# Kernel tuning notes

Hardware: AMD Instinct MI355X
Metric: run time of the kernel (lower is better)

## Reference

```python
import jax, jax.numpy as jnp
import numpy as np
import math

B, CK, CV, H, W = 16, 64, 512, 56, 56


def setup_inputs() -> dict:
    key = jax.random.key(0)
    k1, k2, k3, k4 = jax.random.split(key, 4)
    return {
        "mk": jax.random.normal(k1, (B, CK, H, W), dtype=jnp.float32),
        "qk": jax.random.normal(k2, (B, CK, H, W), dtype=jnp.float32),
        "mv": jax.random.normal(k3, (B, CV, H, W), dtype=jnp.float32),
        "qv": jax.random.normal(k4, (B, CV, H, W), dtype=jnp.float32),
    }


def reference(mk, qk, mv, qv):
    b, ck, h, w = qk.shape
    cv = mv.shape[1]
    n = h * w
    qk_f = qk.reshape(b, ck, n)          # [B, CK, HW] query keys
    mk_f = mk.reshape(b, ck, -1)         # [B, CK, N_mem]
    # squared-L2 affinity (query-norm term is constant per column -> dropped, cancels in softmax)
    a = jnp.sum(mk_f * mk_f, axis=1)[:, :, None]                # [B, N_mem, 1]
    bb = 2.0 * jnp.einsum('bcn,bcm->bnm', mk_f, qk_f)           # [B, N_mem, HW]
    affinity = (-a + bb) / math.sqrt(ck)
    affinity = jax.nn.softmax(affinity, axis=1)                 # softmax over memory dim
    # readout: weighted sum of memory values
    mem = jnp.einsum('bcn,bnm->bcm', mv.reshape(b, cv, -1), affinity)
    mem = mem.reshape(b, cv, h, w)
    return mem, qv
```

## Files before the change

kernel.cpp:

```cpp
#include <hip/hip_runtime.h>


#define B_   16
#define CK_  64
#define CV_  512
#define N_   3136
#define NPAD 3200
#define TM   64
#define TN   128
#define NITER 25
#define NBLK32 100
#define NBLK16 200

typedef __bf16 bf16_t;
typedef bf16_t bf16x8 __attribute__((ext_vector_type(8)));
typedef bf16_t bf16x4 __attribute__((ext_vector_type(4)));
typedef float  f32x16 __attribute__((ext_vector_type(16)));
typedef float  f32x4  __attribute__((ext_vector_type(4)));

#define SCALE_DOT 0.36067376022224085f

__global__ __launch_bounds__(256) void prep_kq(const float* __restrict__ mk,
                                               const float* __restrict__ qk,
                                               bf16_t* __restrict__ Kf,
                                               bf16_t* __restrict__ Qf,
                                               float* __restrict__ a2) {
  int idx = blockIdx.x * 256 + threadIdx.x;
  int b = idx / NPAD, n = idx % NPAD;
  bool valid = n < N_;
  int l32n = n & 31, nblk = n >> 5;
  float ss = 0.f;
  const float* mkp = mk + (size_t)b * CK_ * N_ + n;
  const float* qkp = qk + (size_t)b * CK_ * N_ + n;
  bf16x8* Kf8 = (bf16x8*)Kf;
  bf16x8* Qf8 = (bf16x8*)Qf;
  #pragma unroll
  for (int cc = 0; cc < 8; cc++) {
    bf16x8 kv, qv8;
    #pragma unroll
    for (int j = 0; j < 8; j++) {
      int c = 8 * cc + j;
      float kx = valid ? mkp[(size_t)c * N_] : 0.f;
      float qx = valid ? qkp[(size_t)c * N_] : 0.f;
      ss += kx * kx;
      kv[j] = (bf16_t)kx;
      qv8[j] = (bf16_t)qx;
    }
    int s = cc >> 1, hh = cc & 1;
    size_t pos = (((size_t)b * NBLK32 + nblk) * 4 + s) * 64 + l32n + 32 * hh;
    Kf8[pos] = kv;
    Qf8[pos] = qv8;
  }
  a2[idx] = ss * 0.125f * 1.4426950408889634f;
}

__global__ __launch_bounds__(256) void prep_v(const float* __restrict__ mv,
                                              bf16_t* __restrict__ Vf) {
  int idx = blockIdx.x * 256 + threadIdx.x;
  int lane = idx & 63;
  int t1 = idx >> 6;
  int nblk = t1 % NBLK16;
  int t2 = t1 / NBLK16;
  int cblk = t2 & 15;
  int b = t2 >> 4;
  int c = cblk * 32 + (lane & 31);
  int n = nblk * 16 + (lane >> 5) * 8;
  bf16x8 o;
  if (n < N_) {
    const float* p = mv + ((size_t)b * CV_ + c) * N_ + n;
    f32x4 v0 = *(const f32x4*)p;
    f32x4 v1 = *(const f32x4*)(p + 4);
    #pragma unroll
    for (int j = 0; j < 4; j++) { o[j] = (bf16_t)v0[j]; o[4 + j] = (bf16_t)v1[j]; }
  } else {
    #pragma unroll
    for (int j = 0; j < 8; j++) o[j] = (bf16_t)0.f;
  }
  ((bf16x8*)Vf)[idx] = o;
}

__global__ __launch_bounds__(512) void attn_main(const bf16_t* __restrict__ Kf,
                                                 const bf16_t* __restrict__ Qf,
                                                 const float* __restrict__ a2,
                                                 const bf16_t* __restrict__ Vf,
                                                 float* __restrict__ out) {
  const int xcd = blockIdx.x & 7;
  const int idx = blockIdx.x >> 3;
  const int q49 = idx / 49;
  const int b   = xcd * 2 + q49;
  const int m0  = (idx - q49 * 49) * TM;

  const int tid  = threadIdx.x;
  const int w    = tid >> 6;
  const int lane = tid & 63;
  const int l32  = lane & 31;
  const int h    = lane >> 5;
  const int g    = w >> 2;
  const int i    = w & 3;

  __shared__ __align__(16) bf16_t Plds[2][64][128];
  __shared__ float  Llds[8][32];
  __shared__ float  Linv[64];

  const bf16x8* Qf8 = (const bf16x8*)Qf;
  const int mblk = (m0 >> 5) + g;
  bf16x8 qfrag[4];
  #pragma unroll
  for (int s = 0; s < 4; s++)
    qfrag[s] = Qf8[(((size_t)b * NBLK32 + mblk) * 4 + s) * 64 + lane];

  f32x16 acc[2][2];
  #pragma unroll
  for (int cb = 0; cb < 2; cb++)
    #pragma unroll
    for (int mb = 0; mb < 2; mb++)
      #pragma unroll
      for (int r = 0; r < 16; r++) acc[cb][mb][r] = 0.f;

  float Lpart = 0.f;
  const float*  a2b = a2 + (size_t)b * NPAD;
  const bf16x8* Kf8 = (const bf16x8*)Kf;
  const bf16x8* Vf8 = (const bf16x8*)Vf + (((size_t)b * 16 + 2 * w) * NBLK16) * 64 + lane;

  const int wrow = 32 * g + l32;
  const int wswz = (wrow & 15) << 4;
  const int rswz = (l32 & 15) << 4;

  for (int iter = 0; iter < NITER; iter++) {
    const int n0 = iter * TN + 32 * i;

    f32x16 sacc;
    #pragma unroll
    for (int r = 0; r < 16; r++) sacc[r] = 0.f;
    const bf16x8* kp = Kf8 + (((size_t)b * NBLK32 + (iter * 4 + i)) * 4) * 64 + lane;
    #pragma unroll
    for (int s = 0; s < 4; s++) {
      bf16x8 kf = kp[s * 64];
      sacc = __builtin_amdgcn_mfma_f32_32x32x16_bf16(kf, qfrag[s], sacc, 0, 0, 0);
    }

    char* Pb = (char*)Plds[iter & 1];
    #pragma unroll
    for (int t = 0; t < 4; t++) {
      bf16x4 pk;
      #pragma unroll
      for (int q = 0; q < 4; q++) {
        int r = 8 * t + 4 * h + q;
        int n = n0 + r;
        float vv = sacc[4 * t + q] * SCALE_DOT - a2b[n];
        float p = (n < N_) ? __builtin_amdgcn_exp2f(vv) : 0.f;
        Lpart += p;
        pk[q] = (bf16_t)p;
      }
      int colb = 64 * i + 16 * t + 8 * h;
      *(bf16x4*)(Pb + wrow * 256 + (colb ^ wswz)) = pk;
    }

    __syncthreads();

    const bf16x8* vp = Vf8 + (size_t)iter * 8 * 64;
    #pragma unroll
    for (int t = 0; t < 8; t++) {
      bf16x8 vf0 = vp[t * 64];
      bf16x8 vf1 = vp[t * 64 + 12800];
      bf16x8 pf0 = *(const bf16x8*)(Pb + l32 * 256 + ((32 * t + 16 * h) ^ rswz));
      bf16x8 pf1 = *(const bf16x8*)(Pb + (32 + l32) * 256 + ((32 * t + 16 * h) ^ rswz));
      acc[0][0] = __builtin_amdgcn_mfma_f32_32x32x16_bf16(vf0, pf0, acc[0][0], 0, 0, 0);
      acc[0][1] = __builtin_amdgcn_mfma_f32_32x32x16_bf16(vf0, pf1, acc[0][1], 0, 0, 0);
      acc[1][0] = __builtin_amdgcn_mfma_f32_32x32x16_bf16(vf1, pf0, acc[1][0], 0, 0, 0);
      acc[1][1] = __builtin_amdgcn_mfma_f32_32x32x16_bf16(vf1, pf1, acc[1][1], 0, 0, 0);
    }
  }

  Lpart += __shfl_xor(Lpart, 32, 64);
  if (h == 0) Llds[w][l32] = Lpart;
  __syncthreads();
  if (tid < 64) {
    int gg = tid >> 5;
    float s = 0.f;
    #pragma unroll
    for (int ww = 0; ww < 4; ww++) s += Llds[4 * gg + ww][tid & 31];
    Linv[tid] = 1.0f / s;
  }
  __syncthreads();

  #pragma unroll
  for (int cb = 0; cb < 2; cb++) {
    #pragma unroll
    for (int mb = 0; mb < 2; mb++) {
      float rl = Linv[32 * mb + l32];
      #pragma unroll
      for (int reg = 0; reg < 16; reg++) {
        int r = (reg & 3) + 8 * (reg >> 2) + 4 * h;
        int c = 64 * w + 32 * cb + r;
        out[((size_t)b * CV_ + c) * N_ + m0 + 32 * mb + l32] = acc[cb][mb][reg] * rl;
      }
    }
  }
}

extern "C" void kernel_launch(void* const* d_in, const int* in_sizes, int n_in,
                              void* d_out, int out_size, void* d_ws, size_t ws_size,
                              hipStream_t stream) {
  const float* mk = (const float*)d_in[0];
  const float* qk = (const float*)d_in[1];
  const float* mv = (const float*)d_in[2];
  const float* qv = (const float*)d_in[3];
  float* out = (float*)d_out;

  char* ws = (char*)d_ws;
  bf16_t* Kf = (bf16_t*)(ws);
  bf16_t* Qf = (bf16_t*)(ws + 6553600);
  float*  a2 = (float*)(ws + 13107200);
  bf16_t* Vf = (bf16_t*)(ws + 13312000);

  prep_kq<<<dim3((B_ * NPAD) / 256), dim3(256), 0, stream>>>(mk, qk, Kf, Qf, a2);
  prep_v<<<dim3((B_ * CV_ * NPAD / 8) / 256), dim3(256), 0, stream>>>(mv, Vf);
  attn_main<<<dim3(B_ * 49), dim3(512), 0, stream>>>(Kf, Qf, a2, Vf, out);

  hipMemcpyAsync(out + (size_t)B_ * CV_ * N_, qv,
                 (size_t)B_ * CV_ * N_ * sizeof(float),
                 hipMemcpyDeviceToDevice, stream);
}
```

Baseline: 757.8 us.

## Prefetch K/V tiles per iteration, fold norm bias into MFMA init, coalesce V prep

The attention kernel now issues all K, V and norm-bias loads at the top of each iteration, before the score MFMAs, so global latency overlaps compute. The key-norm term is pre-scaled and used as the initial value of the score accumulator. Padded positions get a huge sentinel, which removes the per-element subtract and bounds check in the softmax. prep_v is rewritten to stage rows through swizzled LDS for coalesced reads and writes, and the qv hipMemcpy is replaced by a vector copy kernel. Costs are higher register pressure from holding 16 V fragments (hence launch_bounds with 2 blocks per CU) and a manual waitcnt plus barrier in place of __syncthreads.

```diff
diff --git a/kernel.cpp b/kernel.cpp
--- a/kernel.cpp
+++ b/kernel.cpp
@@ -17,6 +17,7 @@
 typedef bf16_t bf16x4 __attribute__((ext_vector_type(4)));
 typedef float  f32x16 __attribute__((ext_vector_type(16)));
 typedef float  f32x4  __attribute__((ext_vector_type(4)));
+typedef float  float4_t __attribute__((ext_vector_type(4)));
 
 #define SCALE_DOT 0.36067376022224085f
 
@@ -51,39 +52,69 @@
     Kf8[pos] = kv;
     Qf8[pos] = qv8;
   }
-  a2[idx] = ss * 0.125f * 1.4426950408889634f;
-}
-
+  a2[idx] = valid ? ss * 0.5f : 3.0e38f;
+}
+
+#define VCHUNK 512
 __global__ __launch_bounds__(256) void prep_v(const float* __restrict__ mv,
                                               bf16_t* __restrict__ Vf) {
-  int idx = blockIdx.x * 256 + threadIdx.x;
-  int lane = idx & 63;
-  int t1 = idx >> 6;
-  int nblk = t1 % NBLK16;
-  int t2 = t1 / NBLK16;
+  __shared__ __align__(16) bf16_t T[32][VCHUNK];
+  int wg = blockIdx.x;
+  int chunk = wg % 7;
+  int t2 = wg / 7;
   int cblk = t2 & 15;
   int b = t2 >> 4;
-  int c = cblk * 32 + (lane & 31);
-  int n = nblk * 16 + (lane >> 5) * 8;
-  bf16x8 o;
-  if (n < N_) {
-    const float* p = mv + ((size_t)b * CV_ + c) * N_ + n;
-    f32x4 v0 = *(const f32x4*)p;
-    f32x4 v1 = *(const f32x4*)(p + 4);
-    #pragma unroll
-    for (int j = 0; j < 4; j++) { o[j] = (bf16_t)v0[j]; o[4 + j] = (bf16_t)v1[j]; }
-  } else {
-    #pragma unroll
-    for (int j = 0; j < 8; j++) o[j] = (bf16_t)0.f;
-  }
-  ((bf16x8*)Vf)[idx] = o;
-}
-
-__global__ __launch_bounds__(512) void attn_main(const bf16_t* __restrict__ Kf,
-                                                 const bf16_t* __restrict__ Qf,
-                                                 const float* __restrict__ a2,
-                                                 const bf16_t* __restrict__ Vf,
-                                                 float* __restrict__ out) {
+  int n0 = chunk * VCHUNK;
+  int tid = threadIdx.x;
+
+  const float* base = mv + ((size_t)b * CV_ + cblk * 32) * N_;
+  #pragma unroll
+  for (int rep = 0; rep < 16; rep++) {
+    int idx = rep * 256 + tid;
+    int cl = idx >> 7;
+    int np = (idx & 127) * 4;
+    int n = n0 + np;
+    bf16x4 o;
+    if (n < N_) {
+      f32x4 v = *(const f32x4*)(base + (size_t)cl * N_ + n);
+      #pragma unroll
+      for (int j = 0; j < 4; j++) o[j] = (bf16_t)v[j];
+    } else {
+      #pragma unroll
+      for (int j = 0; j < 4; j++) o[j] = (bf16_t)0.f;
+    }
+    *(bf16x4*)((char*)T + cl * (VCHUNK * 2) + ((np * 2) ^ ((cl & 7) << 4))) = o;
+  }
+  __syncthreads();
+
+  bf16x8* Vf8 = (bf16x8*)Vf;
+  size_t outbase = (((size_t)b * 16 + cblk) * NBLK16 + (n0 >> 4)) * 64;
+  #pragma unroll
+  for (int pass = 0; pass < 8; pass++) {
+    int idx = pass * 256 + tid;
+    int nb = idx >> 6;
+    int ln = idx & 63;
+    if (n0 + nb * 16 < NPAD) {
+      int cl = ln & 31;
+      int n_loc = nb * 16 + (ln >> 5) * 8;
+      bf16x8 o = *(bf16x8*)((char*)T + cl * (VCHUNK * 2) +
+                            ((n_loc * 2) ^ ((cl & 7) << 4)));
+      Vf8[outbase + (size_t)nb * 64 + ln] = o;
+    }
+  }
+}
+
+__global__ __launch_bounds__(256) void copy_qv(const float4_t* __restrict__ src,
+                                               float4_t* __restrict__ dst) {
+  size_t i = (size_t)blockIdx.x * 256 + threadIdx.x;
+  dst[i] = src[i];
+}
+
+__global__ __launch_bounds__(512, 2) void attn_main(const bf16_t* __restrict__ Kf,
+                                                    const bf16_t* __restrict__ Qf,
+                                                    const float* __restrict__ A2S,
+                                                    const bf16_t* __restrict__ Vf,
+                                                    float* __restrict__ out) {
   const int xcd = blockIdx.x & 7;
   const int idx = blockIdx.x >> 3;
   const int q49 = idx / 49;
@@ -118,7 +149,7 @@
       for (int r = 0; r < 16; r++) acc[cb][mb][r] = 0.f;
 
   float Lpart = 0.f;
-  const float*  a2b = a2 + (size_t)b * NPAD;
+  const float*  a2b = A2S + (size_t)b * NPAD;
   const bf16x8* Kf8 = (const bf16x8*)Kf;
   const bf16x8* Vf8 = (const bf16x8*)Vf + (((size_t)b * 16 + 2 * w) * NBLK16) * 64 + lane;
 
@@ -129,15 +160,29 @@
   for (int iter = 0; iter < NITER; iter++) {
     const int n0 = iter * TN + 32 * i;
 
+    const bf16x8* kp = Kf8 + (((size_t)b * NBLK32 + (iter * 4 + i)) * 4) * 64 + lane;
+    bf16x8 kf0 = kp[0], kf1 = kp[64], kf2 = kp[128], kf3 = kp[192];
+    f32x4 na[4];
+    #pragma unroll
+    for (int t = 0; t < 4; t++)
+      na[t] = *(const f32x4*)(a2b + n0 + 8 * t + 4 * h);
+    const bf16x8* vp = Vf8 + (size_t)iter * 8 * 64;
+    bf16x8 vf[16];
+    #pragma unroll
+    for (int t = 0; t < 8; t++) {
+      vf[2 * t]     = vp[t * 64];
+      vf[2 * t + 1] = vp[t * 64 + NBLK16 * 64];
+    }
+
     f32x16 sacc;
     #pragma unroll
-    for (int r = 0; r < 16; r++) sacc[r] = 0.f;
-    const bf16x8* kp = Kf8 + (((size_t)b * NBLK32 + (iter * 4 + i)) * 4) * 64 + lane;
-    #pragma unroll
-    for (int s = 0; s < 4; s++) {
-      bf16x8 kf = kp[s * 64];
-      sacc = __builtin_amdgcn_mfma_f32_32x32x16_bf16(kf, qfrag[s], sacc, 0, 0, 0);
-    }
+    for (int t = 0; t < 4; t++)
+      #pragma unroll
+      for (int q = 0; q < 4; q++) sacc[4 * t + q] = -na[t][q];
+    sacc = __builtin_amdgcn_mfma_f32_32x32x16_bf16(kf0, qfrag[0], sacc, 0, 0, 0);
+    sacc = __builtin_amdgcn_mfma_f32_32x32x16_bf16(kf1, qfrag[1], sacc, 0, 0, 0);
+    sacc = __builtin_amdgcn_mfma_f32_32x32x16_bf16(kf2, qfrag[2], sacc, 0, 0, 0);
+    sacc = __builtin_amdgcn_mfma_f32_32x32x16_bf16(kf3, qfrag[3], sacc, 0, 0, 0);
 
     char* Pb = (char*)Plds[iter & 1];
     #pragma unroll
@@ -145,10 +190,7 @@
       bf16x4 pk;
       #pragma unroll
       for (int q = 0; q < 4; q++) {
-        int r = 8 * t + 4 * h + q;
-        int n = n0 + r;
-        float vv = sacc[4 * t + q] * SCALE_DOT - a2b[n];
-        float p = (n < N_) ? __builtin_amdgcn_exp2f(vv) : 0.f;
+        float p = __builtin_amdgcn_exp2f(sacc[4 * t + q] * SCALE_DOT);
         Lpart += p;
         pk[q] = (bf16_t)p;
       }
@@ -156,19 +198,17 @@
       *(bf16x4*)(Pb + wrow * 256 + (colb ^ wswz)) = pk;
     }
 
-    __syncthreads();
-
-    const bf16x8* vp = Vf8 + (size_t)iter * 8 * 64;
+    asm volatile("s_waitcnt lgkmcnt(0)" ::: "memory");
+    __builtin_amdgcn_s_barrier();
+
     #pragma unroll
     for (int t = 0; t < 8; t++) {
-      bf16x8 vf0 = vp[t * 64];
-      bf16x8 vf1 = vp[t * 64 + 12800];
       bf16x8 pf0 = *(const bf16x8*)(Pb + l32 * 256 + ((32 * t + 16 * h) ^ rswz));
       bf16x8 pf1 = *(const bf16x8*)(Pb + (32 + l32) * 256 + ((32 * t + 16 * h) ^ rswz));
-      acc[0][0] = __builtin_amdgcn_mfma_f32_32x32x16_bf16(vf0, pf0, acc[0][0], 0, 0, 0);
-      acc[0][1] = __builtin_amdgcn_mfma_f32_32x32x16_bf16(vf0, pf1, acc[0][1], 0, 0, 0);
-      acc[1][0] = __builtin_amdgcn_mfma_f32_32x32x16_bf16(vf1, pf0, acc[1][0], 0, 0, 0);
-      acc[1][1] = __builtin_amdgcn_mfma_f32_32x32x16_bf16(vf1, pf1, acc[1][1], 0, 0, 0);
+      acc[0][0] = __builtin_amdgcn_mfma_f32_32x32x16_bf16(vf[2 * t],     pf0, acc[0][0], 0, 0, 0);
+      acc[0][1] = __builtin_amdgcn_mfma_f32_32x32x16_bf16(vf[2 * t],     pf1, acc[0][1], 0, 0, 0);
+      acc[1][0] = __builtin_amdgcn_mfma_f32_32x32x16_bf16(vf[2 * t + 1], pf0, acc[1][0], 0, 0, 0);
+      acc[1][1] = __builtin_amdgcn_mfma_f32_32x32x16_bf16(vf[2 * t + 1], pf1, acc[1][1], 0, 0, 0);
     }
   }
 
@@ -215,10 +255,8 @@
   bf16_t* Vf = (bf16_t*)(ws + 13312000);
 
   prep_kq<<<dim3((B_ * NPAD) / 256), dim3(256), 0, stream>>>(mk, qk, Kf, Qf, a2);
-  prep_v<<<dim3((B_ * CV_ * NPAD / 8) / 256), dim3(256), 0, stream>>>(mv, Vf);
+  prep_v<<<dim3(B_ * 16 * 7), dim3(256), 0, stream>>>(mv, Vf);
   attn_main<<<dim3(B_ * 49), dim3(512), 0, stream>>>(Kf, Qf, a2, Vf, out);
-
-  hipMemcpyAsync(out + (size_t)B_ * CV_ * N_, qv,
-                 (size_t)B_ * CV_ * N_ * sizeof(float),
-                 hipMemcpyDeviceToDevice, stream);
-}
+  copy_qv<<<dim3((B_ * CV_ * N_) / 4 / 256), dim3(256), 0, stream>>>(
+      (const float4_t*)qv, (float4_t*)(out + (size_t)B_ * CV_ * N_));
+}
```

Result: faster. 636.7 us (-16.0%).
